# Optimization experiments

Hardware: AMD Instinct MI355X
Metric: run time of the kernel (lower is better)

## Reference

```python
import jax, jax.numpy as jnp
import numpy as np

N, E, F_IN, H, C = 50000, 800000, 128, 4, 64
NEG_SLOPE = 0.2
LN_EPS = 1e-5


def setup_inputs() -> dict:
    key = jax.random.key(0)
    ks = jax.random.split(key, 8)
    s = 0.05
    return {
        "x": jax.random.normal(ks[0], (N, F_IN), jnp.float32),
        "edge_index": jax.random.randint(ks[1], (2, E), 0, N, jnp.int64).astype(jnp.int32),
        "Wl": jax.random.normal(ks[2], (F_IN, H * C), jnp.float32) * s,
        "bl": jnp.zeros((H * C,), jnp.float32),
        "Wr": jax.random.normal(ks[3], (F_IN, H * C), jnp.float32) * s,
        "br": jnp.zeros((H * C,), jnp.float32),
        "att": jax.random.normal(ks[4], (H, C), jnp.float32) * s,
        "bias_out": jnp.zeros((H * C,), jnp.float32),
        "Wproj": jax.random.normal(ks[5], (H * C, C), jnp.float32) * s,
        "ln_w": jnp.ones((C,), jnp.float32),
        "ln_b": jnp.zeros((C,), jnp.float32),
        "Wres": jax.random.normal(ks[6], (F_IN, C), jnp.float32) * s,
    }


def reference(x, edge_index, Wl, bl, Wr, br, att, bias_out, Wproj, ln_w, ln_b, Wres):
    n = x.shape[0]
    # add self loops (GATv2Conv add_self_loops=True)
    loop = jnp.arange(n, dtype=edge_index.dtype)
    src = jnp.concatenate([edge_index[0], loop])
    dst = jnp.concatenate([edge_index[1], loop])

    xl = (x @ Wl + bl).reshape(n, H, C)  # source-side transform
    xr = (x @ Wr + br).reshape(n, H, C)  # target-side transform

    # GATv2 edge scores: a^T LeakyReLU(xl_j + xr_i)
    m = xl[src] + xr[dst]                              # [Etot, H, C]
    e = jnp.einsum('ehc,hc->eh', jax.nn.leaky_relu(m, NEG_SLOPE), att)

    # segment softmax over incoming edges per destination node
    emax = jax.ops.segment_max(e, dst, num_segments=n)  # every node has a self loop
    ex = jnp.exp(e - emax[dst])
    denom = jax.ops.segment_sum(ex, dst, num_segments=n)
    alpha = ex / denom[dst]                             # [Etot, H]

    # scatter-aggregate messages, concat heads, output bias
    msg = xl[src] * alpha[:, :, None]                   # [Etot, H, C]
    out = jax.ops.segment_sum(msg, dst, num_segments=n).reshape(n, H * C) + bias_out

    # proj -> layernorm -> GELU -> (+ residual); dropout inactive in eval
    out = out @ Wproj                                   # [N, C]
    mu = out.mean(-1, keepdims=True)
    var = jnp.mean(jnp.square(out - mu), -1, keepdims=True)
    out = (out - mu) * jax.lax.rsqrt(var + LN_EPS) * ln_w + ln_b
    out = jax.nn.gelu(out, approximate=False)
    return out + x @ Wres
```

## Files before the change

### kernel.cpp

```cpp
#include <hip/hip_runtime.h>
#include <math.h>

#define NEG_SLOPE 0.2f
#define LN_EPS 1e-5f
#define HC 256
#define NHEAD 4
#define CDIM 64
#define FIN 128
#define CAP 96
#define CSTRIDE 16

typedef short bf16x8 __attribute__((ext_vector_type(8)));
typedef float f32x4  __attribute__((ext_vector_type(4)));

__device__ inline unsigned short f2bf(float f) {
    unsigned u = __builtin_bit_cast(unsigned, f);
    return (unsigned short)((u + 0x7FFFu + ((u >> 16) & 1u)) >> 16);
}
__device__ inline float bf2f(unsigned short s) {
    return __builtin_bit_cast(float, (unsigned)s << 16);
}
__device__ inline void unpack8(const uint4 u, float* f) {
    f[0] = __builtin_bit_cast(float, u.x << 16);
    f[1] = __builtin_bit_cast(float, u.x & 0xffff0000u);
    f[2] = __builtin_bit_cast(float, u.y << 16);
    f[3] = __builtin_bit_cast(float, u.y & 0xffff0000u);
    f[4] = __builtin_bit_cast(float, u.z << 16);
    f[5] = __builtin_bit_cast(float, u.z & 0xffff0000u);
    f[6] = __builtin_bit_cast(float, u.w << 16);
    f[7] = __builtin_bit_cast(float, u.w & 0xffff0000u);
}

__global__ __launch_bounds__(256) void k_prep(
    const float* __restrict__ Wl, const float* __restrict__ Wr,
    const float* __restrict__ Wproj, const float* __restrict__ Wres,
    const float* __restrict__ bias_out, const float* __restrict__ att,
    ushort* __restrict__ wlb, ushort* __restrict__ wrb,
    ushort* __restrict__ wpj, ushort* __restrict__ wrs,
    float* __restrict__ bpj, float* __restrict__ att_s)
{
    const int t = threadIdx.x;
    const int b = blockIdx.x;
    if (b < 224) {
        const int gid = b * 256 + t;
        if (gid < 32768) {
            const int idx = gid;
            const int j = idx & 7, n = (idx >> 3) & 255, q = idx >> 11;
            const int k = (q >> 2) * 32 + (q & 3) * 8 + j;
            wlb[idx] = f2bf(Wl[k * HC + n]);
            wrb[idx] = f2bf(Wr[k * HC + n]);
        } else if (gid < 49152) {
            const int idx = gid - 32768;
            const int j = idx & 7, n = (idx >> 3) & 63, q = idx >> 9;
            const int k = (q >> 2) * 32 + (q & 3) * 8 + j;
            wpj[idx] = f2bf(Wproj[k * CDIM + n]);
        } else {
            const int idx = gid - 49152;
            const int j = idx & 7, n = (idx >> 3) & 63, q = idx >> 9;
            const int k = (q >> 2) * 32 + (q & 3) * 8 + j;
            wrs[idx] = f2bf(Wres[k * CDIM + n]);
        }
    } else {
        att_s[t] = att[t] * 1.44269504088896f;
        __shared__ float part[4][CDIM];
        const int col = t & 63, q = t >> 6;
        float s = 0.f;
        for (int k = q * 64; k < q * 64 + 64; ++k)
            s += bias_out[k] * Wproj[k * CDIM + col];
        part[q][col] = s;
        __syncthreads();
        if (q == 0)
            bpj[col] = part[0][col] + part[1][col] + part[2][col] + part[3][col];
    }
}

__global__ __launch_bounds__(256) void k_main(
    const int* __restrict__ ei,
    int* __restrict__ cnt, int* __restrict__ bucket,
    const float* __restrict__ x,
    const ushort* __restrict__ wlb, const ushort* __restrict__ wrb,
    const float* __restrict__ bl, const float* __restrict__ br,
    ushort* __restrict__ x_bf,
    ushort* __restrict__ xl, ushort* __restrict__ xr,
    int nb_sc, int E, int n_nodes)
{
    const int t = threadIdx.x;

    if (blockIdx.x < nb_sc) {
        const int gid = blockIdx.x * 256 + t;
        if (gid < E) {
            const int s = ei[gid];
            const int d = ei[E + gid];
            const int slot = atomicAdd(&cnt[d * CSTRIDE], 1);
            __builtin_nontemporal_store(s, &bucket[d * CAP + slot]);
        }
        return;
    }

    const int wid = (blockIdx.x - nb_sc) * 4 + (t >> 6);
    const int lane = t & 63;
    const int ntiles = n_nodes >> 4;
    if (wid >= ntiles * 2) return;
    const int side = wid & 1;
    const int tile = wid >> 1;

    const ushort* __restrict__ wb   = side ? wrb : wlb;
    const float*  __restrict__ bias = side ? br : bl;
    ushort*       __restrict__ outp = side ? xr : xl;

    const int m  = lane & 15;
    const int kb = lane >> 4;
    const long arow = ((long)tile * 16 + m) * FIN;

    f32x4 acc[16];
#pragma unroll
    for (int f = 0; f < 16; ++f) acc[f] = (f32x4){0.f, 0.f, 0.f, 0.f};

    for (int ks = 0; ks < 4; ++ks) {
        const float4 lo = *reinterpret_cast<const float4*>(&x[arow + ks * 32 + kb * 8]);
        const float4 hi = *reinterpret_cast<const float4*>(&x[arow + ks * 32 + kb * 8 + 4]);
        union { bf16x8 v; ushort u[8]; } xf;
        xf.u[0] = f2bf(lo.x); xf.u[1] = f2bf(lo.y);
        xf.u[2] = f2bf(lo.z); xf.u[3] = f2bf(lo.w);
        xf.u[4] = f2bf(hi.x); xf.u[5] = f2bf(hi.y);
        xf.u[6] = f2bf(hi.z); xf.u[7] = f2bf(hi.w);
        if (side == 0)
            *reinterpret_cast<bf16x8*>(&x_bf[arow + ks * 32 + kb * 8]) = xf.v;

        const ushort* __restrict__ wq = wb + (size_t)((ks * 4 + kb) * HC) * 8;
#pragma unroll
        for (int f = 0; f < 16; ++f) {
            const bf16x8 wf = *reinterpret_cast<const bf16x8*>(&wq[(f * 16 + m) * 8]);
            acc[f] = __builtin_amdgcn_mfma_f32_16x16x32_bf16(wf, xf.v, acc[f], 0, 0, 0);
        }
    }
    const long obase = ((long)tile * 16 + m) * HC;
#pragma unroll
    for (int f = 0; f < 16; ++f) {
        const int ch = f * 16 + kb * 4;
        const float4 bi = *reinterpret_cast<const float4*>(&bias[ch]);
        ushort4 o;
        o.x = f2bf(acc[f][0] + bi.x);
        o.y = f2bf(acc[f][1] + bi.y);
        o.z = f2bf(acc[f][2] + bi.z);
        o.w = f2bf(acc[f][3] + bi.w);
        *reinterpret_cast<ushort4*>(&outp[obase + ch]) = o;
    }
}

__global__ __launch_bounds__(256) void k_gat_gather(
    const int* __restrict__ cnt, const int* __restrict__ bucket,
    const ushort* __restrict__ xl, const ushort* __restrict__ xr,
    const float* __restrict__ att_s,
    ushort* __restrict__ agg, int n_nodes)
{
    const int node = blockIdx.x * 4 + (threadIdx.x >> 6);
    const int lane = threadIdx.x & 63;
    if (node >= n_nodes) return;

    const int cn = cnt[node * CSTRIDE];
    const int half = lane >> 5;
    const unsigned ch = (unsigned)(lane & 31) * 8;

    float xrv[8], atv[8];
    unpack8(*reinterpret_cast<const uint4*>(&xr[(unsigned)node * HC + ch]), xrv);
    const float4 a0 = *reinterpret_cast<const float4*>(&att_s[ch]);
    const float4 a1 = *reinterpret_cast<const float4*>(&att_s[ch + 4]);
    atv[0] = a0.x; atv[1] = a0.y; atv[2] = a0.z; atv[3] = a0.w;
    atv[4] = a1.x; atv[5] = a1.y; atv[6] = a1.z; atv[7] = a1.w;

    float cs[8];
    unpack8(*reinterpret_cast<const uint4*>(&xl[(unsigned)node * HC + ch]), cs);
    float ps = 0.f;
#pragma unroll
    for (int j = 0; j < 8; ++j) {
        float m = cs[j] + xrv[j];
        m = fmaxf(m, NEG_SLOPE * m);
        ps += m * atv[j];
    }
    ps += __shfl_xor(ps, 1);
    ps += __shfl_xor(ps, 2);
    ps += __shfl_xor(ps, 4);
    float es;
    asm("v_exp_f32 %0, %1" : "=v"(es) : "v"(ps));
    es = (half == 0) ? es : 0.f;
    float den = es;
    float ac[8];
#pragma unroll
    for (int j = 0; j < 8; ++j) ac[j] = es * cs[j];

    if (cn > 0) {
        const int beg = node * CAP;
        const int end = beg + cn;
        const int last = end - 1;

        const int i0 = bucket[min(beg + half, last)];
        const int i1 = bucket[min(beg + 2 + half, last)];
        const int i2 = bucket[min(beg + 4 + half, last)];
        const int i3 = bucket[min(beg + 6 + half, last)];
        int ip = bucket[min(beg + 8 + half, last)];
        int iq = bucket[min(beg + 10 + half, last)];
        uint4 d0 = *reinterpret_cast<const uint4*>(&xl[((unsigned)i0 << 8) + ch]);
        uint4 d1 = *reinterpret_cast<const uint4*>(&xl[((unsigned)i1 << 8) + ch]);
        uint4 d2 = *reinterpret_cast<const uint4*>(&xl[((unsigned)i2 << 8) + ch]);
        uint4 d3 = *reinterpret_cast<const uint4*>(&xl[((unsigned)i3 << 8) + ch]);

        for (int k = beg; k < end; k += 2) {
            const uint4 cu = d0;
            d0 = d1; d1 = d2; d2 = d3;
            d3 = *reinterpret_cast<const uint4*>(&xl[((unsigned)ip << 8) + ch]);
            ip = iq;
            iq = bucket[min(k + 12 + half, last)];

            float c[8];
            unpack8(cu, c);
            float p = 0.f;
#pragma unroll
            for (int j = 0; j < 8; ++j) {
                float m = c[j] + xrv[j];
                m = fmaxf(m, NEG_SLOPE * m);
                p += m * atv[j];
            }
            p += __shfl_xor(p, 1);
            p += __shfl_xor(p, 2);
            p += __shfl_xor(p, 4);

            float e;
            asm("v_exp_f32 %0, %1" : "=v"(e) : "v"(p));
            e = (k + half < end) ? e : 0.f;
            den += e;
#pragma unroll
            for (int j = 0; j < 8; ++j) ac[j] += e * c[j];
        }
    }

    den += __shfl_xor(den, 32);
#pragma unroll
    for (int j = 0; j < 8; ++j) ac[j] += __shfl_xor(ac[j], 32);

    if (lane < 32) {
        const float inv = 1.f / den;
        uint4 o;
        o.x = ((unsigned)f2bf(ac[1] * inv) << 16) | f2bf(ac[0] * inv);
        o.y = ((unsigned)f2bf(ac[3] * inv) << 16) | f2bf(ac[2] * inv);
        o.z = ((unsigned)f2bf(ac[5] * inv) << 16) | f2bf(ac[4] * inv);
        o.w = ((unsigned)f2bf(ac[7] * inv) << 16) | f2bf(ac[6] * inv);
        *reinterpret_cast<uint4*>(&agg[(unsigned)node * HC + ch]) = o;
    }
}

__global__ __launch_bounds__(256) void k_post_mfma(
    const ushort* __restrict__ aggb, const ushort* __restrict__ xb,
    const ushort* __restrict__ wpj, const ushort* __restrict__ wrs,
    const float* __restrict__ bpj,
    const float* __restrict__ ln_w, const float* __restrict__ ln_b,
    float* __restrict__ out, int n_nodes)
{
    const int wid = blockIdx.x * 4 + (threadIdx.x >> 6);
    const int lane = threadIdx.x & 63;
    const int ntiles = n_nodes >> 4;
    if (wid >= ntiles) return;

    const int m  = lane & 15;
    const int kb = lane >> 4;
    const long node = (long)wid * 16 + m;
    const long gbase = node * HC;
    const long xbase = node * FIN;

    f32x4 ap[4], ar[4];
#pragma unroll
    for (int f = 0; f < 4; ++f) {
        ap[f] = (f32x4){0.f, 0.f, 0.f, 0.f};
        ar[f] = (f32x4){0.f, 0.f, 0.f, 0.f};
    }

    for (int ks = 0; ks < 8; ++ks) {
        const bf16x8 af = *reinterpret_cast<const bf16x8*>(&aggb[gbase + ks * 32 + kb * 8]);
        const ushort* __restrict__ wq = wpj + (size_t)((ks * 4 + kb) * CDIM) * 8;
#pragma unroll
        for (int f = 0; f < 4; ++f) {
            const bf16x8 wf = *reinterpret_cast<const bf16x8*>(&wq[(f * 16 + m) * 8]);
            ap[f] = __builtin_amdgcn_mfma_f32_16x16x32_bf16(wf, af, ap[f], 0, 0, 0);
        }
    }
    for (int ks = 0; ks < 4; ++ks) {
        const bf16x8 af = *reinterpret_cast<const bf16x8*>(&xb[xbase + ks * 32 + kb * 8]);
        const ushort* __restrict__ wq = wrs + (size_t)((ks * 4 + kb) * CDIM) * 8;
#pragma unroll
        for (int f = 0; f < 4; ++f) {
            const bf16x8 wf = *reinterpret_cast<const bf16x8*>(&wq[(f * 16 + m) * 8]);
            ar[f] = __builtin_amdgcn_mfma_f32_16x16x32_bf16(wf, af, ar[f], 0, 0, 0);
        }
    }

    float p[4][4];
#pragma unroll
    for (int f = 0; f < 4; ++f) {
        const float4 bp = *reinterpret_cast<const float4*>(&bpj[f * 16 + kb * 4]);
#pragma unroll
        for (int j = 0; j < 4; ++j) p[f][j] = ap[f][j] + ((const float*)&bp)[j];
    }

    float s1 = 0.f;
#pragma unroll
    for (int f = 0; f < 4; ++f)
#pragma unroll
        for (int j = 0; j < 4; ++j) s1 += p[f][j];
    s1 += __shfl_xor(s1, 16); s1 += __shfl_xor(s1, 32);
    const float mu = s1 * (1.f / 64.f);

    float s2 = 0.f;
#pragma unroll
    for (int f = 0; f < 4; ++f)
#pragma unroll
        for (int j = 0; j < 4; ++j) {
            const float d = p[f][j] - mu;
            s2 += d * d;
        }
    s2 += __shfl_xor(s2, 16); s2 += __shfl_xor(s2, 32);
    const float rs = rsqrtf(s2 * (1.f / 64.f) + LN_EPS);

#pragma unroll
    for (int f = 0; f < 4; ++f) {
        const int ch = f * 16 + kb * 4;
        const float4 lw = *reinterpret_cast<const float4*>(&ln_w[ch]);
        const float4 lb = *reinterpret_cast<const float4*>(&ln_b[ch]);
        float4 ov;
#pragma unroll
        for (int j = 0; j < 4; ++j) {
            const float v = (p[f][j] - mu) * rs * ((const float*)&lw)[j] + ((const float*)&lb)[j];
            const float g = 0.5f * v * (1.f + erff(v * 0.70710678118654752f));
            ((float*)&ov)[j] = g + ar[f][j];
        }
        *reinterpret_cast<float4*>(&out[node * CDIM + ch]) = ov;
    }
}

extern "C" void kernel_launch(void* const* d_in, const int* in_sizes, int n_in,
                              void* d_out, int out_size, void* d_ws, size_t ws_size,
                              hipStream_t stream)
{
    const float* x        = (const float*)d_in[0];
    const int*   ei       = (const int*)  d_in[1];
    const float* Wl       = (const float*)d_in[2];
    const float* bl       = (const float*)d_in[3];
    const float* Wr       = (const float*)d_in[4];
    const float* br       = (const float*)d_in[5];
    const float* att      = (const float*)d_in[6];
    const float* bias_out = (const float*)d_in[7];
    const float* Wproj    = (const float*)d_in[8];
    const float* ln_w     = (const float*)d_in[9];
    const float* ln_b     = (const float*)d_in[10];
    const float* Wres     = (const float*)d_in[11];
    float* out = (float*)d_out;

    const int N = in_sizes[0] / FIN;
    const int E = in_sizes[1] / 2;
    const int ntiles = N >> 4;

    ushort* us = (ushort*)d_ws;
    size_t uo = 0;
    ushort* xl_bf  = us + uo; uo += (size_t)N * HC;
    ushort* xr_bf  = us + uo; uo += (size_t)N * HC;
    ushort* agg_bf = us + uo; uo += (size_t)N * HC;
    ushort* x_bf   = us + uo; uo += (size_t)N * FIN;
    ushort* wlb    = us + uo; uo += 32768;
    ushort* wrb    = us + uo; uo += 32768;
    ushort* wpj    = us + uo; uo += 16384;
    ushort* wrs    = us + uo; uo += 8192;
    float* bpj   = (float*)(us + uo);
    float* att_s = bpj + CDIM;
    int* cnt    = (int*)(att_s + HC);
    int* bucket = cnt + (size_t)N * CSTRIDE;

    hipMemsetAsync(cnt, 0, (size_t)N * CSTRIDE * sizeof(int), stream);

    k_prep<<<225, 256, 0, stream>>>(Wl, Wr, Wproj, Wres, bias_out, att,
                                    wlb, wrb, wpj, wrs, bpj, att_s);

    {
        const int nb_sc  = (E + 255) / 256;
        const int nb_lin = (2 * ntiles + 3) / 4;
        k_main<<<nb_sc + nb_lin, 256, 0, stream>>>(
            ei, cnt, bucket, x, wlb, wrb, bl, br,
            x_bf, xl_bf, xr_bf, nb_sc, E, N);
    }

    k_gat_gather<<<(N + 3) / 4, 256, 0, stream>>>(
        cnt, bucket, xl_bf, xr_bf, att_s, agg_bf, N);

    k_post_mfma<<<(ntiles + 3) / 4, 256, 0, stream>>>(
        agg_bf, x_bf, wpj, wrs, bpj, ln_w, ln_b, out, N);
}
```

Baseline: 229.9 us.

## Split edge bucketing into two-pass coarse/fine scatter and separate linear kernel

Replaces the single-pass per-node atomic bucketing (padded counters, fused with the linear transform) with a two-pass scheme. Edges are first scattered into coarse buckets of 8 destination nodes with one global atomic per edge. A second kernel then distributes each coarse bucket into per-node buckets using shared-memory atomics and writes compact per-node counts. This is meant to reduce global atomic contention and cut the memset size, at the cost of an extra kernel launch and an intermediate int2 buffer. Coarse buckets are capped at 256 entries with overflow silently dropped, and the linear MFMA kernel now runs on its own instead of overlapping with the scatter.

After: 212.2 us. 1.08x faster.

```diff
diff --git a/kernel.cpp b/kernel.cpp
--- a/kernel.cpp
+++ b/kernel.cpp
@@ -8,7 +8,7 @@
 #define CDIM 64
 #define FIN 128
 #define CAP 96
-#define CSTRIDE 16
+#define CCAP 256
 
 typedef short bf16x8 __attribute__((ext_vector_type(8)));
 typedef float f32x4  __attribute__((ext_vector_type(4)));
@@ -74,31 +74,51 @@
     }
 }
 
-__global__ __launch_bounds__(256) void k_main(
-    const int* __restrict__ ei,
-    int* __restrict__ cnt, int* __restrict__ bucket,
+__global__ __launch_bounds__(256) void k_scatterA(
+    const int* __restrict__ ei, int* __restrict__ ccnt, int2* __restrict__ cbkt,
+    int E)
+{
+    const int gid = blockIdx.x * 256 + threadIdx.x;
+    if (gid < E) {
+        const int s = ei[gid];
+        const int d = ei[E + gid];
+        const int cb = d >> 3;
+        const int slot = atomicAdd(&ccnt[cb], 1);
+        cbkt[(size_t)cb * CCAP + slot] = make_int2(d, s);
+    }
+}
+
+__global__ __launch_bounds__(256) void k_scatterB(
+    const int* __restrict__ ccnt, const int2* __restrict__ cbkt,
+    int* __restrict__ cnt, int* __restrict__ bucket, int n_nodes)
+{
+    __shared__ int lcnt[8];
+    const int t = threadIdx.x;
+    const int b = blockIdx.x;
+    if (t < 8) lcnt[t] = 0;
+    __syncthreads();
+    const int n = min(ccnt[b], CCAP);
+    for (int i = t; i < n; i += 256) {
+        const int2 p = cbkt[(size_t)b * CCAP + i];
+        const int slot = atomicAdd(&lcnt[p.x & 7], 1);
+        bucket[p.x * CAP + slot] = p.y;
+    }
+    __syncthreads();
+    if (t < 8) {
+        const int d = b * 8 + t;
+        if (d < n_nodes) cnt[d] = lcnt[t];
+    }
+}
+
+__global__ __launch_bounds__(256) void k_linear_mfma(
     const float* __restrict__ x,
     const ushort* __restrict__ wlb, const ushort* __restrict__ wrb,
     const float* __restrict__ bl, const float* __restrict__ br,
     ushort* __restrict__ x_bf,
-    ushort* __restrict__ xl, ushort* __restrict__ xr,
-    int nb_sc, int E, int n_nodes)
-{
-    const int t = threadIdx.x;
-
-    if (blockIdx.x < nb_sc) {
-        const int gid = blockIdx.x * 256 + t;
-        if (gid < E) {
-            const int s = ei[gid];
-            const int d = ei[E + gid];
-            const int slot = atomicAdd(&cnt[d * CSTRIDE], 1);
-            __builtin_nontemporal_store(s, &bucket[d * CAP + slot]);
-        }
-        return;
-    }
-
-    const int wid = (blockIdx.x - nb_sc) * 4 + (t >> 6);
-    const int lane = t & 63;
+    ushort* __restrict__ xl, ushort* __restrict__ xr, int n_nodes)
+{
+    const int wid = blockIdx.x * 4 + (threadIdx.x >> 6);
+    const int lane = threadIdx.x & 63;
     const int ntiles = n_nodes >> 4;
     if (wid >= ntiles * 2) return;
     const int side = wid & 1;
@@ -158,7 +178,7 @@
     const int lane = threadIdx.x & 63;
     if (node >= n_nodes) return;
 
-    const int cn = cnt[node * CSTRIDE];
+    const int cn = cnt[node];
     const int half = lane >> 5;
     const unsigned ch = (unsigned)(lane & 31) * 8;
 
@@ -357,6 +377,7 @@
     const int N = in_sizes[0] / FIN;
     const int E = in_sizes[1] / 2;
     const int ntiles = N >> 4;
+    const int NCB = (N + 7) >> 3;
 
     ushort* us = (ushort*)d_ws;
     size_t uo = 0;
@@ -371,20 +392,20 @@
     float* bpj   = (float*)(us + uo);
     float* att_s = bpj + CDIM;
     int* cnt    = (int*)(att_s + HC);
-    int* bucket = cnt + (size_t)N * CSTRIDE;
-
-    hipMemsetAsync(cnt, 0, (size_t)N * CSTRIDE * sizeof(int), stream);
+    int* ccnt   = cnt + N;
+    int* bucket = ccnt + NCB;
+    int2* cbkt  = (int2*)(bucket + (size_t)N * CAP);
+
+    hipMemsetAsync(ccnt, 0, (size_t)NCB * sizeof(int), stream);
 
     k_prep<<<225, 256, 0, stream>>>(Wl, Wr, Wproj, Wres, bias_out, att,
                                     wlb, wrb, wpj, wrs, bpj, att_s);
 
-    {
-        const int nb_sc  = (E + 255) / 256;
-        const int nb_lin = (2 * ntiles + 3) / 4;
-        k_main<<<nb_sc + nb_lin, 256, 0, stream>>>(
-            ei, cnt, bucket, x, wlb, wrb, bl, br,
-            x_bf, xl_bf, xr_bf, nb_sc, E, N);
-    }
+    k_scatterA<<<(E + 255) / 256, 256, 0, stream>>>(ei, ccnt, cbkt, E);
+    k_scatterB<<<NCB, 256, 0, stream>>>(ccnt, cbkt, cnt, bucket, N);
+
+    k_linear_mfma<<<(2 * ntiles + 3) / 4, 256, 0, stream>>>(
+        x, wlb, wrb, bl, br, x_bf, xl_bf, xr_bf, N);
 
     k_gat_gather<<<(N + 3) / 4, 256, 0, stream>>>(
         cnt, bucket, xl_bf, xr_bf, att_s, agg_bf, N);
```
